# Optimization experiments

Measured on AMD Instinct MI355X. Metric: run time of the kernel, lower is better.

Reference implementation:

```python
import jax, jax.numpy as jnp
import numpy as np

B = 256      # number of graphs
IN = 128     # input_dim
FD = 256     # feature_dim (dims[1])
HID = 256    # hidden_dim of attention block (dims[2])
OUT = 128    # final output dim (dims[3])
TXT = 512    # text_emb_dim

LENGTHS = np.asarray(128 + (np.arange(B) % 256), dtype=np.int64)  # ragged lens 128..383
N = int(LENGTHS.sum())  # 65408 total nodes
LMAX = int(LENGTHS.max())  # 383


def setup_inputs() -> dict:
    key = jax.random.key(0)
    ks = jax.random.split(key, 16)
    s = 0.02
    return {
        "input": jax.random.normal(ks[0], (N, IN), jnp.float32),
        "text_emb": jax.random.normal(ks[1], (B, TXT), jnp.float32),
        "repeat_list": jnp.asarray(LENGTHS),
        # layer 0: Linear(IN -> FD)
        "W0": jax.random.normal(ks[2], (IN, FD), jnp.float32) * s,
        "b0": jax.random.normal(ks[3], (FD,), jnp.float32) * s,
        # cross-attention block params
        "Wq": jax.random.normal(ks[4], (TXT, FD), jnp.float32) * s,
        "bq": jax.random.normal(ks[5], (FD,), jnp.float32) * s,
        "Wk": jax.random.normal(ks[6], (FD, FD), jnp.float32) * s,
        "bk": jax.random.normal(ks[7], (FD,), jnp.float32) * s,
        "Wv": jax.random.normal(ks[8], (FD, FD), jnp.float32) * s,
        "bv": jax.random.normal(ks[9], (FD,), jnp.float32) * s,
        "Wo": jax.random.normal(ks[10], (FD, HID), jnp.float32) * s,
        "bo": jax.random.normal(ks[11], (HID,), jnp.float32) * s,
        # layer 2: Linear(HID -> OUT), last layer (no activation)
        "W2": jax.random.normal(ks[12], (HID, OUT), jnp.float32) * s,
        "b2": jax.random.normal(ks[13], (OUT,), jnp.float32) * s,
    }


def _cross_attention(h, text_emb, repeat_list, Wq, bq, Wk, bk, Wv, bv, Wo, bo):
    # h: [N, FD] packed ragged node features; repeat_list: [B] lengths (constant ints)
    n = h.shape[0]
    b = repeat_list.shape[0]
    fd = h.shape[1]
    # pad ragged -> [B, LMAX, FD] (pad value 0) + validity mask
    seg = jnp.repeat(jnp.arange(b), repeat_list, total_repeat_length=n)  # [N] graph id
    offsets = jnp.cumsum(repeat_list) - repeat_list                      # [B] start of each graph
    pos = jnp.arange(n) - offsets[seg]                                   # [N] within-graph pos
    padded = jnp.zeros((b, LMAX, fd), h.dtype).at[seg, pos].set(h)
    valid = jnp.arange(LMAX)[None, :] < repeat_list[:, None]             # [B, L]

    q = text_emb @ Wq + bq                              # [B, FD]
    k = (padded @ Wk + bk) * valid[..., None]           # masked_fill(mask==0, 0)
    v = (padded @ Wv + bv) * valid[..., None]

    # query is broadcast identically over the padded-length axis, so each row of the
    # [L, L] score matrix is the same vector: scores[b, j] = q[b] . k[b, j]
    scores = jnp.einsum('bf,bjf->bj', q, k)             # [B, L]
    scores = jnp.where(valid, scores, -jnp.inf)         # mask invalid columns j
    p = jax.nn.softmax(scores, axis=-1)                 # [B, L]
    # output = attention^T @ value with identical rows => out[b,j,:] = p[b,j] * sum_i v[b,i,:]
    v_sum = v.sum(axis=1)                               # [B, FD] (padded rows already zero)
    out_pad = p[..., None] * v_sum[:, None, :]          # [B, L, FD]
    out_nodes = out_pad[seg, pos]                       # unpad-concat -> [N, FD]
    return out_nodes @ Wo + bo                          # [N, HID]


def reference(input, text_emb, repeat_list, W0, b0, Wq, bq, Wk, bk, Wv, bv, Wo, bo, W2, b2):
    h = jax.nn.relu(input @ W0 + b0)                                     # layer 0 + relu
    h = _cross_attention(h, text_emb, repeat_list, Wq, bq, Wk, bk, Wv, bv, Wo, bo)
    h = jax.nn.relu(h)                                                   # layer 1 + relu
    return h @ W2 + b2                                                   # layer 2 (last, no act)
```

## Files before the change

### kernel.cpp

```cpp
#include <hip/hip_runtime.h>
#include <math.h>

#define B_G   256
#define IN_D  128
#define FD    256
#define HID   256
#define OUT_D 128
#define TXT   512
#define NTILES 511
#define XKS   136

typedef short bf16x8 __attribute__((ext_vector_type(8)));
typedef float f32x4  __attribute__((ext_vector_type(4)));

__device__ __forceinline__ f32x4 MFMA(bf16x8 a, bf16x8 b, f32x4 c) {
    return __builtin_amdgcn_mfma_f32_16x16x32_bf16(a, b, c, 0, 0, 0);
}

__device__ __forceinline__ unsigned bf_rne(float x) {
    unsigned u = __float_as_uint(x);
    u += 0x7fffu + ((u >> 16) & 1u);
    return u >> 16;
}
__device__ __forceinline__ float bf_to_f(unsigned h) {
    return __uint_as_float(h << 16);
}
__device__ __forceinline__ bf16x8 pack_hi8(const float4& v0, const float4& v1) {
    uint4 h;
    h.x = bf_rne(v0.x) | (bf_rne(v0.y) << 16);
    h.y = bf_rne(v0.z) | (bf_rne(v0.w) << 16);
    h.z = bf_rne(v1.x) | (bf_rne(v1.y) << 16);
    h.w = bf_rne(v1.z) | (bf_rne(v1.w) << 16);
    return __builtin_bit_cast(bf16x8, h);
}
__device__ __forceinline__ void split8hl(const float4& v0, const float4& v1,
                                         bf16x8& hf, bf16x8& lf) {
    float a[8] = {v0.x, v0.y, v0.z, v0.w, v1.x, v1.y, v1.z, v1.w};
    uint4 h, l;
    unsigned hh[8], ll[8];
#pragma unroll
    for (int i = 0; i < 8; i++) {
        hh[i] = bf_rne(a[i]);
        ll[i] = bf_rne(a[i] - bf_to_f(hh[i]));
    }
    h.x = hh[0] | (hh[1] << 16); h.y = hh[2] | (hh[3] << 16);
    h.z = hh[4] | (hh[5] << 16); h.w = hh[6] | (hh[7] << 16);
    l.x = ll[0] | (ll[1] << 16); l.y = ll[2] | (ll[3] << 16);
    l.z = ll[4] | (ll[5] << 16); l.w = ll[6] | (ll[7] << 16);
    hf = __builtin_bit_cast(bf16x8, h);
    lf = __builtin_bit_cast(bf16x8, l);
}

__global__ __launch_bounds__(256) void k_wsplit(
    const float* __restrict__ W0, const float* __restrict__ W2,
    const float* __restrict__ Wq, const float* __restrict__ Wv,
    const float* __restrict__ Wo,
    unsigned short* __restrict__ W0H, unsigned short* __restrict__ W0L,
    unsigned short* __restrict__ W2H, unsigned short* __restrict__ W2L,
    unsigned short* __restrict__ WqH, unsigned short* __restrict__ WqL,
    unsigned short* __restrict__ WvH, unsigned short* __restrict__ WvL,
    unsigned short* __restrict__ WoH, unsigned short* __restrict__ WoL)
{
    int blk = blockIdx.x, c = threadIdx.x;
    const float* W; unsigned short* H; unsigned short* L; int N, kc;
    if (blk < 4)       { W = W0; H = W0H; L = W0L; N = 256; kc = blk; }
    else if (blk < 12) { W = W2; H = W2H; L = W2L; N = 128; kc = blk - 4; }
    else if (blk < 28) { W = Wq; H = WqH; L = WqL; N = 256; kc = blk - 12; }
    else if (blk < 36) { W = Wv; H = WvH; L = WvL; N = 256; kc = blk - 28; }
    else               { W = Wo; H = WoH; L = WoL; N = 256; kc = blk - 36; }
    if (c >= N) return;

    unsigned hw[16], lw[16];
#pragma unroll
    for (int kk = 0; kk < 32; kk++) {
        float v = W[(size_t)(kc * 32 + kk) * N + c];
        unsigned h = bf_rne(v);
        unsigned l = bf_rne(v - bf_to_f(h));
        if (kk & 1) { hw[kk >> 1] |= h << 16; lw[kk >> 1] |= l << 16; }
        else        { hw[kk >> 1] = h;        lw[kk >> 1] = l; }
    }
    size_t o = ((size_t)kc * N + c) * 32;
    uint4* hp = (uint4*)(H + o);
    uint4* lp = (uint4*)(L + o);
#pragma unroll
    for (int r = 0; r < 4; r++) {
        hp[r] = make_uint4(hw[r * 4], hw[r * 4 + 1], hw[r * 4 + 2], hw[r * 4 + 3]);
        lp[r] = make_uint4(lw[r * 4], lw[r * 4 + 1], lw[r * 4 + 2], lw[r * 4 + 3]);
    }
}

__global__ __launch_bounds__(256) void k_prep(
    const float* __restrict__ X, const int* __restrict__ lens,
    unsigned short* __restrict__ Xbf, int* __restrict__ offsets,
    float* __restrict__ hsum, float* __restrict__ scores)
{
    int blk = blockIdx.x, tid = threadIdx.x;
    if (blk < NTILES) {
        size_t base = (size_t)blk * 16384;
#pragma unroll
        for (int it = 0; it < 8; it++) {
            size_t off = base + it * 2048 + tid * 8;
            const float4* p = (const float4*)(X + off);
            float4 v0 = p[0], v1 = p[1];
            *(uint4*)(Xbf + off) = __builtin_bit_cast(uint4, pack_hi8(v0, v1));
        }
        if (tid < 128) {
            hsum[blk * 128 + tid] = 0.f;
            scores[blk * 128 + tid] = 0.f;
        }
    } else {
        if (tid < 128) hsum[511 * 128 + tid] = 0.f;
        __shared__ int sc[B_G];
        sc[tid] = lens[tid];
        __syncthreads();
        for (int d = 1; d < 256; d <<= 1) {
            int v = (tid >= d) ? sc[tid - d] : 0;
            __syncthreads();
            sc[tid] += v;
            __syncthreads();
        }
        offsets[tid + 1] = sc[tid];
        if (tid == 0) offsets[0] = 0;
    }
}

__global__ __launch_bounds__(256) void k_q(
    const float* __restrict__ TE,
    const unsigned short* __restrict__ WqH, const unsigned short* __restrict__ WqL,
    const float* __restrict__ bq, float* __restrict__ q)
{
    int blk = blockIdx.x;
    int rbase = (blk >> 2) * 64, cbase = (blk & 3) * 64;
    int tid = threadIdx.x, lane = tid & 63, w = tid >> 6;
    int ln = lane & 15, quad = lane >> 4;

    f32x4 acc[4] = {};
    int arow = rbase + w * 16 + ln;
#pragma unroll
    for (int kc = 0; kc < 16; kc++) {
        const float4* ap = (const float4*)(TE + (size_t)arow * TXT + kc * 32 + quad * 8);
        bf16x8 AH, AL;
        split8hl(ap[0], ap[1], AH, AL);
#pragma unroll
        for (int j = 0; j < 4; j++) {
            int c = cbase + 16 * j + ln;
            size_t bo = ((size_t)kc * 256 + c) * 32 + quad * 8;
            bf16x8 BH = *(const bf16x8*)(WqH + bo);
            bf16x8 BL = *(const bf16x8*)(WqL + bo);
            acc[j] = MFMA(AH, BH, acc[j]);
            acc[j] = MFMA(AH, BL, acc[j]);
            acc[j] = MFMA(AL, BH, acc[j]);
        }
    }
#pragma unroll
    for (int j = 0; j < 4; j++) {
        int c = cbase + 16 * j + ln;
        float bb = bq[c];
#pragma unroll
        for (int r = 0; r < 4; r++) {
            int row = rbase + w * 16 + quad * 4 + r;
            q[(size_t)row * FD + c] = acc[j][r] + bb;
        }
    }
}

__global__ __launch_bounds__(256) void k_qk(
    const float* __restrict__ q, const float* __restrict__ Wk,
    float* __restrict__ qk)
{
    int blk = blockIdx.x;
    int rbase = (blk >> 2) * 64, cbase = (blk & 3) * 64;
    int tid = threadIdx.x, lane = tid & 63, w = tid >> 6;
    int ln = lane & 15, quad = lane >> 4;

    f32x4 acc[4] = {};
    int arow = rbase + w * 16 + ln;
#pragma unroll
    for (int kc = 0; kc < 8; kc++) {
        const float4* ap = (const float4*)(q + (size_t)arow * FD + kc * 32 + quad * 8);
        bf16x8 AH, AL;
        split8hl(ap[0], ap[1], AH, AL);
#pragma unroll
        for (int j = 0; j < 4; j++) {
            int f = cbase + 16 * j + ln;
            const float4* bp = (const float4*)(Wk + (size_t)f * FD + kc * 32 + quad * 8);
            bf16x8 BH, BL;
            split8hl(bp[0], bp[1], BH, BL);
            acc[j] = MFMA(AH, BH, acc[j]);
            acc[j] = MFMA(AH, BL, acc[j]);
            acc[j] = MFMA(AL, BH, acc[j]);
        }
    }
#pragma unroll
    for (int j = 0; j < 4; j++) {
        int f = cbase + 16 * j + ln;
#pragma unroll
        for (int r = 0; r < 4; r++) {
            int row = rbase + w * 16 + quad * 4 + r;
            qk[(size_t)row * FD + f] = acc[j][r];
        }
    }
}

__global__ __launch_bounds__(256) void k_l0(
    const unsigned short* __restrict__ Xbf,
    const unsigned short* __restrict__ W0H, const unsigned short* __restrict__ W0L,
    const float* __restrict__ b0, const float* __restrict__ qk,
    const int* __restrict__ offsets,
    float* __restrict__ scores, float* __restrict__ hsum)
{
    int t = blockIdx.y, bx = blockIdx.x;
    int n0 = t * 128;
    int tid = threadIdx.x, lane = tid & 63, w = tid >> 6;
    int ln = lane & 15, quad = lane >> 4;
    int i2 = w & 1, j2 = w >> 1;

    __shared__ __align__(16) unsigned short Xs[128 * XKS];
    __shared__ int offs[257];
    __shared__ float qks[2][128];
    __shared__ float bsh[128];

    offs[tid] = offsets[tid];
    if (tid == 0) offs[256] = offsets[256];
    __syncthreads();

    int lo = 0, hi = 255;
#pragma unroll
    for (int s = 0; s < 8; s++) {
        int mid = (lo + hi + 1) >> 1;
        if (offs[mid] <= n0) lo = mid; else hi = mid - 1;
    }
    int g0 = lo;
    lo = g0; hi = 255;
#pragma unroll
    for (int s = 0; s < 8; s++) {
        int mid = (lo + hi + 1) >> 1;
        if (offs[mid] <= n0 + 127) lo = mid; else hi = mid - 1;
    }
    int g1 = lo;
    int boundary = (g1 > g0) ? offs[g1] : 0x7fffffff;

    if (tid < 128) {
        bsh[tid] = b0[bx * 128 + tid];
        qks[0][tid] = qk[(size_t)g0 * FD + bx * 128 + tid];
        qks[1][tid] = qk[(size_t)g1 * FD + bx * 128 + tid];
    }
#pragma unroll
    for (int it = 0; it < 8; it++) {
        int row = it * 16 + (tid >> 4);
        int kq = (tid & 15) * 8;
        *(uint4*)(Xs + row * XKS + kq) =
            *(const uint4*)(Xbf + (size_t)(n0 + row) * IN_D + kq);
    }
    __syncthreads();

    f32x4 acc[4][4] = {};
#pragma unroll
    for (int kc = 0; kc < 4; kc++) {
        bf16x8 AH[4], BH[4], BL[4];
#pragma unroll
        for (int i = 0; i < 4; i++)
            AH[i] = *(const bf16x8*)(Xs + (i2 * 64 + 16 * i + ln) * XKS + kc * 32 + quad * 8);
#pragma unroll
        for (int j = 0; j < 4; j++) {
            int c = bx * 128 + j2 * 64 + 16 * j + ln;
            size_t bo = ((size_t)kc * 256 + c) * 32 + quad * 8;
            BH[j] = *(const bf16x8*)(W0H + bo);
            BL[j] = *(const bf16x8*)(W0L + bo);
        }
#pragma unroll
        for (int i = 0; i < 4; i++)
#pragma unroll
            for (int j = 0; j < 4; j++) {
                acc[i][j] = MFMA(AH[i], BH[j], acc[i][j]);
                acc[i][j] = MFMA(AH[i], BL[j], acc[i][j]);
            }
    }

    float sp[4][4];
    float cs[4][2];
#pragma unroll
    for (int i = 0; i < 4; i++)
#pragma unroll
        for (int r = 0; r < 4; r++) sp[i][r] = 0.f;
#pragma unroll
    for (int j = 0; j < 4; j++) { cs[j][0] = 0.f; cs[j][1] = 0.f; }

#pragma unroll
    for (int i = 0; i < 4; i++)
#pragma unroll
        for (int j = 0; j < 4; j++) {
            int cl = j2 * 64 + 16 * j + ln;
            float bb = bsh[cl];
#pragma unroll
            for (int r = 0; r < 4; r++) {
                int node = i2 * 64 + 16 * i + quad * 4 + r;
                int gb = (n0 + node >= boundary) ? 1 : 0;
                float h = fmaxf(acc[i][j][r] + bb, 0.f);
                sp[i][r] = fmaf(h, qks[gb][cl], sp[i][r]);
                cs[j][gb] += h;
            }
        }
#pragma unroll
    for (int i = 0; i < 4; i++)
#pragma unroll
        for (int r = 0; r < 4; r++) {
            float s = sp[i][r];
            s += __shfl_xor(s, 1); s += __shfl_xor(s, 2);
            s += __shfl_xor(s, 4); s += __shfl_xor(s, 8);
            if (ln == 0) {
                int node = i2 * 64 + 16 * i + quad * 4 + r;
                atomicAdd(&scores[n0 + node], s);
            }
        }
#pragma unroll
    for (int j = 0; j < 4; j++) {
        int cl = j2 * 64 + 16 * j + ln;
#pragma unroll
        for (int gb = 0; gb < 2; gb++) {
            float s = cs[j][gb];
            s += __shfl_xor(s, 16); s += __shfl_xor(s, 32);
            if (quad == 0 && (gb == 0 || g1 > g0)) {
                int g = gb ? g1 : g0;
                atomicAdd(&hsum[(size_t)g * FD + bx * 128 + cl], s);
            }
        }
    }
}

__global__ __launch_bounds__(256) void k_mid(
    const float* __restrict__ scores, const float* __restrict__ hsum,
    const unsigned short* __restrict__ WvH, const unsigned short* __restrict__ WvL,
    const float* __restrict__ bv,
    const unsigned short* __restrict__ WoH, const unsigned short* __restrict__ WoL,
    const int* __restrict__ offsets,
    float* __restrict__ wvec, float* __restrict__ smax, float* __restrict__ dinv)
{
    int blk = blockIdx.x, tid = threadIdx.x;
    if (blk < 4) {
        __shared__ float vs[64 * 260];
        __shared__ int offs2[65];
        int base = blk * 64;
        int lane = tid & 63, w = tid >> 6;
        int ln = lane & 15, quad = lane >> 4;
        if (tid < 65) offs2[tid] = offsets[base + tid];
        __syncthreads();

        f32x4 acc[4][4] = {};
#pragma unroll
        for (int kc = 0; kc < 8; kc++) {
            bf16x8 AH[4], AL[4], BH[4], BL[4];
#pragma unroll
            for (int i = 0; i < 4; i++) {
                const float4* ap = (const float4*)(hsum + (size_t)(base + 16 * i + ln) * FD + kc * 32 + quad * 8);
                split8hl(ap[0], ap[1], AH[i], AL[i]);
            }
#pragma unroll
            for (int j = 0; j < 4; j++) {
                int c = w * 64 + 16 * j + ln;
                size_t bo = ((size_t)kc * 256 + c) * 32 + quad * 8;
                BH[j] = *(const bf16x8*)(WvH + bo);
                BL[j] = *(const bf16x8*)(WvL + bo);
            }
#pragma unroll
            for (int i = 0; i < 4; i++)
#pragma unroll
                for (int j = 0; j < 4; j++) {
                    acc[i][j] = MFMA(AH[i], BH[j], acc[i][j]);
                    acc[i][j] = MFMA(AH[i], BL[j], acc[i][j]);
                    acc[i][j] = MFMA(AL[i], BH[j], acc[i][j]);
                }
        }
#pragma unroll
        for (int i = 0; i < 4; i++)
#pragma unroll
            for (int j = 0; j < 4; j++) {
                int c = w * 64 + 16 * j + ln;
                float bvc = bv[c];
#pragma unroll
                for (int r = 0; r < 4; r++) {
                    int row = 16 * i + quad * 4 + r;
                    float len = (float)(offs2[row + 1] - offs2[row]);
                    vs[row * 260 + c] = acc[i][j][r] + len * bvc;
                }
            }
        __syncthreads();

        f32x4 acc2[4][4] = {};
#pragma unroll
        for (int kc = 0; kc < 8; kc++) {
            bf16x8 AH[4], AL[4], BH[4], BL[4];
#pragma unroll
            for (int i = 0; i < 4; i++) {
                const float4* ap = (const float4*)(vs + (16 * i + ln) * 260 + kc * 32 + quad * 8);
                split8hl(ap[0], ap[1], AH[i], AL[i]);
            }
#pragma unroll
            for (int j = 0; j < 4; j++) {
                int c = w * 64 + 16 * j + ln;
                size_t bo = ((size_t)kc * 256 + c) * 32 + quad * 8;
                BH[j] = *(const bf16x8*)(WoH + bo);
                BL[j] = *(const bf16x8*)(WoL + bo);
            }
#pragma unroll
            for (int i = 0; i < 4; i++)
#pragma unroll
                for (int j = 0; j < 4; j++) {
                    acc2[i][j] = MFMA(AH[i], BH[j], acc2[i][j]);
                    acc2[i][j] = MFMA(AH[i], BL[j], acc2[i][j]);
                    acc2[i][j] = MFMA(AL[i], BH[j], acc2[i][j]);
                }
        }
#pragma unroll
        for (int i = 0; i < 4; i++)
#pragma unroll
            for (int j = 0; j < 4; j++) {
                int c = w * 64 + 16 * j + ln;
#pragma unroll
                for (int r = 0; r < 4; r++) {
                    int row = 16 * i + quad * 4 + r;
                    wvec[(size_t)(base + row) * HID + c] = acc2[i][j][r];
                }
            }
    } else {
        int b = blk - 4;
        int off = offsets[b], len = offsets[b + 1] - off;
        __shared__ float redm[4], reds[4];
        float m = -INFINITY;
        for (int i = tid; i < len; i += 256) m = fmaxf(m, scores[off + i]);
        for (int d = 1; d < 64; d <<= 1) m = fmaxf(m, __shfl_xor(m, d));
        if ((tid & 63) == 0) redm[tid >> 6] = m;
        __syncthreads();
        m = fmaxf(fmaxf(redm[0], redm[1]), fmaxf(redm[2], redm[3]));
        float s = 0.f;
        for (int i = tid; i < len; i += 256) s += expf(scores[off + i] - m);
        for (int d = 1; d < 64; d <<= 1) s += __shfl_xor(s, d);
        if ((tid & 63) == 0) reds[tid >> 6] = s;
        __syncthreads();
        if (tid == 0) {
            smax[b] = m;
            dinv[b] = 1.0f / (reds[0] + reds[1] + reds[2] + reds[3]);
        }
    }
}

__global__ __launch_bounds__(256) void k_fin(
    const float* __restrict__ scores, const float* __restrict__ wvec,
    const float* __restrict__ bo,
    const unsigned short* __restrict__ W2H, const unsigned short* __restrict__ W2L,
    const float* __restrict__ b2, const float* __restrict__ smax,
    const float* __restrict__ dinv, const int* __restrict__ offsets,
    float* __restrict__ Y)
{
    int t = blockIdx.x;
    int n0 = t * 128;
    int tid = threadIdx.x, lane = tid & 63, w = tid >> 6;
    int ln = lane & 15, quad = lane >> 4;
    int i2 = w & 1, j2 = w >> 1;

    __shared__ int offs[257];
    __shared__ float wsh[2][HID];
    __shared__ float bosh[HID];
    __shared__ float b2sh[OUT_D];
    __shared__ float sd[4];

    offs[tid] = offsets[tid];
    if (tid == 0) offs[256] = offsets[256];
    __syncthreads();

    int lo = 0, hi = 255;
#pragma unroll
    for (int s = 0; s < 8; s++) {
        int mid = (lo + hi + 1) >> 1;
        if (offs[mid] <= n0) lo = mid; else hi = mid - 1;
    }
    int g0 = lo;
    lo = g0; hi = 255;
#pragma unroll
    for (int s = 0; s < 8; s++) {
        int mid = (lo + hi + 1) >> 1;
        if (offs[mid] <= n0 + 127) lo = mid; else hi = mid - 1;
    }
    int g1 = lo;
    int boundary = (g1 > g0) ? offs[g1] : 0x7fffffff;

    wsh[0][tid] = wvec[(size_t)g0 * HID + tid];
    wsh[1][tid] = wvec[(size_t)g1 * HID + tid];
    bosh[tid] = bo[tid];
    if (tid < OUT_D) b2sh[tid] = b2[tid];
    if (tid == 0) { sd[0] = smax[g0]; sd[1] = dinv[g0]; sd[2] = smax[g1]; sd[3] = dinv[g1]; }
    __syncthreads();

    float p[4];
    int gb_i[4];
#pragma unroll
    for (int i = 0; i < 4; i++) {
        int node = i2 * 64 + 16 * i + ln;
        int gb = (n0 + node >= boundary) ? 1 : 0;
        gb_i[i] = gb;
        p[i] = expf(scores[n0 + node] - sd[gb * 2]) * sd[gb * 2 + 1];
    }

    f32x4 acc[4][4] = {};
#pragma unroll
    for (int kc = 0; kc < 8; kc++) {
        float4 bo0 = *(const float4*)&bosh[kc * 32 + quad * 8];
        float4 bo1 = *(const float4*)&bosh[kc * 32 + quad * 8 + 4];
        bf16x8 AH[4], BH[4], BL[4];
#pragma unroll
        for (int i = 0; i < 4; i++) {
            float4 wv0 = *(const float4*)&wsh[gb_i[i]][kc * 32 + quad * 8];
            float4 wv1 = *(const float4*)&wsh[gb_i[i]][kc * 32 + quad * 8 + 4];
            float4 z0, z1;
            z0.x = fmaxf(fmaf(p[i], wv0.x, bo0.x), 0.f);
            z0.y = fmaxf(fmaf(p[i], wv0.y, bo0.y), 0.f);
            z0.z = fmaxf(fmaf(p[i], wv0.z, bo0.z), 0.f);
            z0.w = fmaxf(fmaf(p[i], wv0.w, bo0.w), 0.f);
            z1.x = fmaxf(fmaf(p[i], wv1.x, bo1.x), 0.f);
            z1.y = fmaxf(fmaf(p[i], wv1.y, bo1.y), 0.f);
            z1.z = fmaxf(fmaf(p[i], wv1.z, bo1.z), 0.f);
            z1.w = fmaxf(fmaf(p[i], wv1.w, bo1.w), 0.f);
            AH[i] = pack_hi8(z0, z1);
        }
#pragma unroll
        for (int j = 0; j < 4; j++) {
            int c = j2 * 64 + 16 * j + ln;
            size_t boff = ((size_t)kc * 128 + c) * 32 + quad * 8;
            BH[j] = *(const bf16x8*)(W2H + boff);
            BL[j] = *(const bf16x8*)(W2L + boff);
        }
#pragma unroll
        for (int i = 0; i < 4; i++)
#pragma unroll
            for (int j = 0; j < 4; j++) {
                acc[i][j] = MFMA(AH[i], BH[j], acc[i][j]);
                acc[i][j] = MFMA(AH[i], BL[j], acc[i][j]);
            }
    }

#pragma unroll
    for (int i = 0; i < 4; i++)
#pragma unroll
        for (int j = 0; j < 4; j++) {
            int c = j2 * 64 + 16 * j + ln;
            float bb = b2sh[c];
#pragma unroll
            for (int r = 0; r < 4; r++) {
                int node = i2 * 64 + 16 * i + quad * 4 + r;
                Y[(size_t)(n0 + node) * OUT_D + c] = acc[i][j][r] + bb;
            }
        }
}

extern "C" void kernel_launch(void* const* d_in, const int* in_sizes, int n_in,
                              void* d_out, int out_size, void* d_ws, size_t ws_size,
                              hipStream_t stream)
{
    const float* X        = (const float*)d_in[0];
    const float* text_emb = (const float*)d_in[1];
    const int*   lens     = (const int*)d_in[2];
    const float* W0       = (const float*)d_in[3];
    const float* b0       = (const float*)d_in[4];
    const float* Wq       = (const float*)d_in[5];
    const float* bq       = (const float*)d_in[6];
    const float* Wk       = (const float*)d_in[7];
    const float* Wv       = (const float*)d_in[9];
    const float* bv       = (const float*)d_in[10];
    const float* Wo       = (const float*)d_in[11];
    const float* bo       = (const float*)d_in[12];
    const float* W2       = (const float*)d_in[13];
    const float* b2       = (const float*)d_in[14];
    float* Y = (float*)d_out;

    char* base = (char*)d_ws;
    size_t o = 0;
    int*   offsets = (int*)(base + o);                  o += 4096;
    float* qbuf    = (float*)(base + o);                o += 262144;
    float* qkbuf   = (float*)(base + o);                o += 262144;
    float* wvec    = (float*)(base + o);                o += 262144;
    float* smaxb   = (float*)(base + o);                o += 1024;
    float* dinvb   = (float*)(base + o);                o += 1024;
    float* hsum    = (float*)(base + o);                o += 262144;
    float* scores  = (float*)(base + o);                o += 262144;
    unsigned short* WqH = (unsigned short*)(base + o);  o += 262144;
    unsigned short* WqL = (unsigned short*)(base + o);  o += 262144;
    unsigned short* WvH = (unsigned short*)(base + o);  o += 131072;
    unsigned short* WvL = (unsigned short*)(base + o);  o += 131072;
    unsigned short* WoH = (unsigned short*)(base + o);  o += 131072;
    unsigned short* WoL = (unsigned short*)(base + o);  o += 131072;
    unsigned short* W0H = (unsigned short*)(base + o);  o += 65536;
    unsigned short* W0L = (unsigned short*)(base + o);  o += 65536;
    unsigned short* W2H = (unsigned short*)(base + o);  o += 65536;
    unsigned short* W2L = (unsigned short*)(base + o);  o += 65536;
    unsigned short* Xbf = (unsigned short*)(base + o);  o += 16744448;

    k_wsplit<<<44, 256, 0, stream>>>(W0, W2, Wq, Wv, Wo,
                                     W0H, W0L, W2H, W2L, WqH, WqL,
                                     WvH, WvL, WoH, WoL);
    k_prep<<<512, 256, 0, stream>>>(X, lens, Xbf, offsets, hsum, scores);
    k_q<<<16, 256, 0, stream>>>(text_emb, WqH, WqL, bq, qbuf);
    k_qk<<<16, 256, 0, stream>>>(qbuf, Wk, qkbuf);
    k_l0<<<dim3(2, NTILES), 256, 0, stream>>>(Xbf, W0H, W0L, b0, qkbuf, offsets, scores, hsum);
    k_mid<<<260, 256, 0, stream>>>(scores, hsum, WvH, WvL, bv, WoH, WoL, offsets,
                                   wvec, smaxb, dinvb);
    k_fin<<<NTILES, 256, 0, stream>>>(scores, wvec, bo, W2H, W2L, b2, smaxb, dinvb,
                                      offsets, Y);
}
```

Baseline: 228.4 us.

## Replace final MFMA GEMM with per-graph piecewise-linear lookup tables over p

Each node's output is relu(p*w_b + bo) @ W2 + b2, which is piecewise linear in the scalar p with breakpoints at -bo/w. A new per-graph kernel sorts the breakpoints and builds a prefix table of (A,B) coefficient pairs, so each node only binary-searches its interval and computes Y = p*A + B. This removes the per-node 256x128 matmul in exchange for building a roughly 67 MB table per call, with a serial 256-step loop per graph, plus a gather-heavy output kernel. It also drops the bf16 split of W2.

```diff
diff --git a/kernel.cpp b/kernel.cpp
--- a/kernel.cpp
+++ b/kernel.cpp
@@ -52,34 +52,30 @@
 }
 
 __global__ __launch_bounds__(256) void k_wsplit(
-    const float* __restrict__ W0, const float* __restrict__ W2,
-    const float* __restrict__ Wq, const float* __restrict__ Wv,
-    const float* __restrict__ Wo,
+    const float* __restrict__ W0, const float* __restrict__ Wq,
+    const float* __restrict__ Wv, const float* __restrict__ Wo,
     unsigned short* __restrict__ W0H, unsigned short* __restrict__ W0L,
-    unsigned short* __restrict__ W2H, unsigned short* __restrict__ W2L,
     unsigned short* __restrict__ WqH, unsigned short* __restrict__ WqL,
     unsigned short* __restrict__ WvH, unsigned short* __restrict__ WvL,
     unsigned short* __restrict__ WoH, unsigned short* __restrict__ WoL)
 {
     int blk = blockIdx.x, c = threadIdx.x;
-    const float* W; unsigned short* H; unsigned short* L; int N, kc;
-    if (blk < 4)       { W = W0; H = W0H; L = W0L; N = 256; kc = blk; }
-    else if (blk < 12) { W = W2; H = W2H; L = W2L; N = 128; kc = blk - 4; }
-    else if (blk < 28) { W = Wq; H = WqH; L = WqL; N = 256; kc = blk - 12; }
-    else if (blk < 36) { W = Wv; H = WvH; L = WvL; N = 256; kc = blk - 28; }
-    else               { W = Wo; H = WoH; L = WoL; N = 256; kc = blk - 36; }
-    if (c >= N) return;
+    const float* W; unsigned short* H; unsigned short* L; int kc;
+    if (blk < 4)       { W = W0; H = W0H; L = W0L; kc = blk; }
+    else if (blk < 20) { W = Wq; H = WqH; L = WqL; kc = blk - 4; }
+    else if (blk < 28) { W = Wv; H = WvH; L = WvL; kc = blk - 20; }
+    else               { W = Wo; H = WoH; L = WoL; kc = blk - 28; }
 
     unsigned hw[16], lw[16];
 #pragma unroll
     for (int kk = 0; kk < 32; kk++) {
-        float v = W[(size_t)(kc * 32 + kk) * N + c];
+        float v = W[(size_t)(kc * 32 + kk) * 256 + c];
         unsigned h = bf_rne(v);
         unsigned l = bf_rne(v - bf_to_f(h));
         if (kk & 1) { hw[kk >> 1] |= h << 16; lw[kk >> 1] |= l << 16; }
         else        { hw[kk >> 1] = h;        lw[kk >> 1] = l; }
     }
-    size_t o = ((size_t)kc * N + c) * 32;
+    size_t o = ((size_t)kc * 256 + c) * 32;
     uint4* hp = (uint4*)(H + o);
     uint4* lp = (uint4*)(L + o);
 #pragma unroll
@@ -444,24 +440,86 @@
     }
 }
 
-__global__ __launch_bounds__(256) void k_fin(
-    const float* __restrict__ scores, const float* __restrict__ wvec,
-    const float* __restrict__ bo,
-    const unsigned short* __restrict__ W2H, const unsigned short* __restrict__ W2L,
-    const float* __restrict__ b2, const float* __restrict__ smax,
+__global__ __launch_bounds__(256) void k_tab(
+    const float* __restrict__ wvec, const float* __restrict__ bo,
+    const float* __restrict__ W2, const float* __restrict__ b2,
+    float2* __restrict__ Ttab, float* __restrict__ tsort)
+{
+    int b = blockIdx.x, tid = threadIdx.x;
+    __shared__ float wsh[256], bosh[256];
+    __shared__ unsigned long long key[256];
+    __shared__ unsigned char act[256];
+    __shared__ float partA[2][128], partB[2][128];
+
+    float w = wvec[(size_t)b * HID + tid];
+    float bv = bo[tid];
+    wsh[tid] = w; bosh[tid] = bv;
+
+    int cls;
+    float t = 0.f;
+    if (w > 0.f)      { t = -bv / w; cls = (t <= 0.f) ? 1 : (t >= 1.f ? 0 : 2); }
+    else if (w < 0.f) { t = -bv / w; cls = (t <= 0.f) ? 0 : (t >= 1.f ? 1 : 3); }
+    else              { cls = (bv > 0.f) ? 1 : 0; }
+    unsigned kb = (cls >= 2) ? __float_as_uint(t) : 0x7f800000u;
+    key[tid] = ((unsigned long long)kb << 32) | ((unsigned)cls << 16) | (unsigned)tid;
+    act[tid] = (cls == 1 || cls == 3) ? 1 : 0;
+    __syncthreads();
+
+    for (int k2 = 2; k2 <= 256; k2 <<= 1) {
+        for (int jj = k2 >> 1; jj > 0; jj >>= 1) {
+            __syncthreads();
+            int ixj = tid ^ jj;
+            if (ixj > tid) {
+                bool up = ((tid & k2) == 0);
+                unsigned long long a = key[tid], c2 = key[ixj];
+                if (up ? (a > c2) : (a < c2)) { key[tid] = c2; key[ixj] = a; }
+            }
+        }
+    }
+    __syncthreads();
+    tsort[(size_t)b * 256 + tid] = __uint_as_float((unsigned)(key[tid] >> 32));
+
+    int g = tid >> 7, c = tid & 127;
+    float A = 0.f, Bv = (g == 0) ? b2[c] : 0.f;
+    for (int kk = 128 * g; kk < 128 * g + 128; kk++) {
+        float m = act[kk] ? 1.f : 0.f;
+        float wc = W2[(size_t)kk * OUT_D + c] * m;
+        A = fmaf(wsh[kk], wc, A);
+        Bv = fmaf(bosh[kk], wc, Bv);
+    }
+    partA[g][c] = A; partB[g][c] = Bv;
+    __syncthreads();
+
+    if (tid < 128) {
+        float Aa = partA[0][tid] + partA[1][tid];
+        float Bb = partB[0][tid] + partB[1][tid];
+        size_t rb = (size_t)b * 257 * 128;
+        Ttab[rb + tid] = make_float2(Aa, Bb);
+        for (int j = 1; j <= 256; j++) {
+            unsigned long long kk = key[j - 1];
+            if ((unsigned)(kk >> 32) >= 0x7f800000u) break;
+            float s = (((kk >> 16) & 0xffffu) == 2u) ? 1.f : -1.f;
+            int id = (int)(kk & 0xffffu);
+            float wc = W2[(size_t)id * OUT_D + tid] * s;
+            Aa = fmaf(wsh[id], wc, Aa);
+            Bb = fmaf(bosh[id], wc, Bb);
+            Ttab[rb + (size_t)j * 128 + tid] = make_float2(Aa, Bb);
+        }
+    }
+}
+
+__global__ __launch_bounds__(256) void k_out(
+    const float* __restrict__ scores, const float* __restrict__ tsort,
+    const float2* __restrict__ Ttab, const float* __restrict__ smax,
     const float* __restrict__ dinv, const int* __restrict__ offsets,
     float* __restrict__ Y)
 {
-    int t = blockIdx.x;
-    int n0 = t * 128;
-    int tid = threadIdx.x, lane = tid & 63, w = tid >> 6;
-    int ln = lane & 15, quad = lane >> 4;
-    int i2 = w & 1, j2 = w >> 1;
+    int tt = blockIdx.x;
+    int n0 = tt * 128;
+    int tid = threadIdx.x;
 
     __shared__ int offs[257];
-    __shared__ float wsh[2][HID];
-    __shared__ float bosh[HID];
-    __shared__ float b2sh[OUT_D];
+    __shared__ float ts[2][256];
     __shared__ float sd[4];
 
     offs[tid] = offsets[tid];
@@ -484,72 +542,36 @@
     int g1 = lo;
     int boundary = (g1 > g0) ? offs[g1] : 0x7fffffff;
 
-    wsh[0][tid] = wvec[(size_t)g0 * HID + tid];
-    wsh[1][tid] = wvec[(size_t)g1 * HID + tid];
-    bosh[tid] = bo[tid];
-    if (tid < OUT_D) b2sh[tid] = b2[tid];
+    ts[0][tid] = tsort[(size_t)g0 * 256 + tid];
+    ts[1][tid] = tsort[(size_t)g1 * 256 + tid];
     if (tid == 0) { sd[0] = smax[g0]; sd[1] = dinv[g0]; sd[2] = smax[g1]; sd[3] = dinv[g1]; }
     __syncthreads();
 
-    float p[4];
-    int gb_i[4];
-#pragma unroll
-    for (int i = 0; i < 4; i++) {
-        int node = i2 * 64 + 16 * i + ln;
-        int gb = (n0 + node >= boundary) ? 1 : 0;
-        gb_i[i] = gb;
-        p[i] = expf(scores[n0 + node] - sd[gb * 2]) * sd[gb * 2 + 1];
-    }
-
-    f32x4 acc[4][4] = {};
-#pragma unroll
-    for (int kc = 0; kc < 8; kc++) {
-        float4 bo0 = *(const float4*)&bosh[kc * 32 + quad * 8];
-        float4 bo1 = *(const float4*)&bosh[kc * 32 + quad * 8 + 4];
-        bf16x8 AH[4], BH[4], BL[4];
-#pragma unroll
-        for (int i = 0; i < 4; i++) {
-            float4 wv0 = *(const float4*)&wsh[gb_i[i]][kc * 32 + quad * 8];
-            float4 wv1 = *(const float4*)&wsh[gb_i[i]][kc * 32 + quad * 8 + 4];
-            float4 z0, z1;
-            z0.x = fmaxf(fmaf(p[i], wv0.x, bo0.x), 0.f);
-            z0.y = fmaxf(fmaf(p[i], wv0.y, bo0.y), 0.f);
-            z0.z = fmaxf(fmaf(p[i], wv0.z, bo0.z), 0.f);
-            z0.w = fmaxf(fmaf(p[i], wv0.w, bo0.w), 0.f);
-            z1.x = fmaxf(fmaf(p[i], wv1.x, bo1.x), 0.f);
-            z1.y = fmaxf(fmaf(p[i], wv1.y, bo1.y), 0.f);
-            z1.z = fmaxf(fmaf(p[i], wv1.z, bo1.z), 0.f);
-            z1.w = fmaxf(fmaf(p[i], wv1.w, bo1.w), 0.f);
-            AH[i] = pack_hi8(z0, z1);
-        }
-#pragma unroll
-        for (int j = 0; j < 4; j++) {
-            int c = j2 * 64 + 16 * j + ln;
-            size_t boff = ((size_t)kc * 128 + c) * 32 + quad * 8;
-            BH[j] = *(const bf16x8*)(W2H + boff);
-            BL[j] = *(const bf16x8*)(W2L + boff);
-        }
-#pragma unroll
-        for (int i = 0; i < 4; i++)
-#pragma unroll
-            for (int j = 0; j < 4; j++) {
-                acc[i][j] = MFMA(AH[i], BH[j], acc[i][j]);
-                acc[i][j] = MFMA(AH[i], BL[j], acc[i][j]);
-            }
-    }
-
-#pragma unroll
-    for (int i = 0; i < 4; i++)
-#pragma unroll
-        for (int j = 0; j < 4; j++) {
-            int c = j2 * 64 + 16 * j + ln;
-            float bb = b2sh[c];
-#pragma unroll
-            for (int r = 0; r < 4; r++) {
-                int node = i2 * 64 + 16 * i + quad * 4 + r;
-                Y[(size_t)(n0 + node) * OUT_D + c] = acc[i][j][r] + bb;
-            }
-        }
+    int half = tid & 1, nl = tid >> 1;
+    int node = n0 + nl;
+    int gb = (node >= boundary) ? 1 : 0;
+    float p = expf(scores[node] - sd[gb * 2]) * sd[gb * 2 + 1];
+
+    int j = 0;
+#pragma unroll
+    for (int step = 128; step >= 1; step >>= 1) {
+        int cand = j + step;
+        if (cand <= 256 && ts[gb][cand - 1] <= p) j = cand;
+    }
+
+    const float4* row = (const float4*)(Ttab + ((size_t)(gb ? g1 : g0) * 257 + j) * 128 + half * 64);
+    float4* yrow = (float4*)(Y + (size_t)node * OUT_D + half * 64);
+#pragma unroll
+    for (int u = 0; u < 16; u++) {
+        float4 a = row[2 * u];
+        float4 bq4 = row[2 * u + 1];
+        float4 y;
+        y.x = fmaf(p, a.x, a.y);
+        y.y = fmaf(p, a.z, a.w);
+        y.z = fmaf(p, bq4.x, bq4.y);
+        y.w = fmaf(p, bq4.z, bq4.w);
+        yrow[u] = y;
+    }
 }
 
 extern "C" void kernel_launch(void* const* d_in, const int* in_sizes, int n_in,
@@ -590,19 +612,18 @@
     unsigned short* WoL = (unsigned short*)(base + o);  o += 131072;
     unsigned short* W0H = (unsigned short*)(base + o);  o += 65536;
     unsigned short* W0L = (unsigned short*)(base + o);  o += 65536;
-    unsigned short* W2H = (unsigned short*)(base + o);  o += 65536;
-    unsigned short* W2L = (unsigned short*)(base + o);  o += 65536;
     unsigned short* Xbf = (unsigned short*)(base + o);  o += 16744448;
-
-    k_wsplit<<<44, 256, 0, stream>>>(W0, W2, Wq, Wv, Wo,
-                                     W0H, W0L, W2H, W2L, WqH, WqL,
-                                     WvH, WvL, WoH, WoL);
+    float* tsortb  = (float*)(base + o);                o += 262144;
+    float2* Ttab   = (float2*)(base + o);               o += (size_t)256 * 257 * 128 * 8;
+
+    k_wsplit<<<36, 256, 0, stream>>>(W0, Wq, Wv, Wo,
+                                     W0H, W0L, WqH, WqL, WvH, WvL, WoH, WoL);
     k_prep<<<512, 256, 0, stream>>>(X, lens, Xbf, offsets, hsum, scores);
     k_q<<<16, 256, 0, stream>>>(text_emb, WqH, WqL, bq, qbuf);
     k_qk<<<16, 256, 0, stream>>>(qbuf, Wk, qkbuf);
     k_l0<<<dim3(2, NTILES), 256, 0, stream>>>(Xbf, W0H, W0L, b0, qkbuf, offsets, scores, hsum);
     k_mid<<<260, 256, 0, stream>>>(scores, hsum, WvH, WvL, bv, WoH, WoL, offsets,
                                    wvec, smaxb, dinvb);
-    k_fin<<<NTILES, 256, 0, stream>>>(scores, wvec, bo, W2H, W2L, b2, smaxb, dinvb,
-                                      offsets, Y);
-}
+    k_tab<<<256, 256, 0, stream>>>(wvec, bo, W2, b2, Ttab, tsortb);
+    k_out<<<NTILES, 256, 0, stream>>>(scores, tsortb, Ttab, smaxb, dinvb, offsets, Y);
+}
```

New measurement: 292.7 us. +28.2%, slower.
